# Kernel tuning notes

Hardware: AMD Instinct MI355X
Metric: run time of the kernel (lower is better)

The kernel has to match this reference:

```python
import jax, jax.numpy as jnp
import numpy as np

SIM_THRESHOLD = 0.7
EPS = 1e-8  # matches torch F.cosine_similarity eps

Q, M, D, C = 4096, 65536, 384, 128


def setup_inputs() -> dict:
    key = jax.random.key(0)
    k1, k2, k3 = jax.random.split(key, 3)
    query_embeddings = jax.random.normal(k1, (Q, D), dtype=jnp.float32)
    memory_embeddings = jax.random.normal(k2, (M, D), dtype=jnp.float32)
    # per-example one-hot-ish label vectors [M, C]
    memory_labels = jax.random.uniform(k3, (M, C), dtype=jnp.float32)
    return {
        "query_embeddings": query_embeddings,
        "memory_embeddings": memory_embeddings,
        "memory_labels": memory_labels,
    }


def _l2_normalize(x):
    n = jnp.sqrt(jnp.sum(x * x, axis=-1, keepdims=True))
    return x / jnp.maximum(n, EPS)


def reference(query_embeddings, memory_embeddings, memory_labels):
    # cosine similarity matrix [Q, M] via normalized GEMM
    qn = _l2_normalize(query_embeddings)          # [Q, D]
    mn = _l2_normalize(memory_embeddings)         # [M, D]
    sims = jnp.einsum("qd,md->qm", qn, mn)        # [Q, M]
    max_sim = jnp.max(sims, axis=1)               # [Q]
    max_idx = jnp.argmax(sims, axis=1)            # [Q]
    picked = memory_labels[max_idx]               # [Q, C] gather
    C_ = memory_labels.shape[1]
    uniform = jnp.full((1, C_), 1.0 / C_, dtype=picked.dtype)
    predictions = jnp.where((max_sim > SIM_THRESHOLD)[:, None], picked, uniform)
    return predictions
```

## Files before the change

### kernel.cpp

```cpp
#include <hip/hip_runtime.h>
#include <math.h>

#define QN 4096
#define MN 65536
#define DN 384
#define CN 128
#define NCHUNK 64
#define MROWS_PER_CHUNK (MN / NCHUNK)
#define MT_PER (MROWS_PER_CHUNK / 64)

#define LROW 400
#define LCHUNKS 25
#define BTILE_B (64 * LROW)
#define GTILE_B (64 * DN)

typedef __attribute__((ext_vector_type(8))) int i32x8;
typedef __attribute__((ext_vector_type(4))) int i32x4;
typedef __attribute__((ext_vector_type(4))) float f32x4;

__device__ __forceinline__ unsigned char f2fp8(float f) {
  return (unsigned char)(__builtin_amdgcn_cvt_pk_fp8_f32(f, 0.f, 0, false) & 0xff);
}

__device__ __forceinline__ void async16(const void* g, void* l) {
  __builtin_amdgcn_global_load_lds(
      (const __attribute__((address_space(1))) unsigned int*)g,
      (__attribute__((address_space(3))) unsigned int*)l, 16, 0, 0);
}

__global__ __launch_bounds__(256) void nrm_kernel(const float* __restrict__ qe,
                                                  const float* __restrict__ me,
                                                  unsigned char* __restrict__ yq,
                                                  unsigned char* __restrict__ ym) {
  const int row = blockIdx.x * 4 + (threadIdx.x >> 6);
  const int lane = threadIdx.x & 63;
  const float* xr;
  unsigned char* yr;
  if (row < QN) {
    xr = qe + (size_t)row * DN;
    yr = yq + (size_t)row * DN;
  } else {
    xr = me + (size_t)(row - QN) * DN;
    yr = ym + (size_t)(row - QN) * DN;
  }
  float v[6];
  float ss = 0.f;
#pragma unroll
  for (int i = 0; i < 6; ++i) {
    v[i] = xr[lane + i * 64];
    ss += v[i] * v[i];
  }
#pragma unroll
  for (int m = 1; m < 64; m <<= 1) ss += __shfl_xor(ss, m);
  const float scale = 1.0f / fmaxf(sqrtf(ss), 1e-8f);
#pragma unroll
  for (int i = 0; i < 6; ++i) yr[lane + i * 64] = f2fp8(v[i] * scale);
}

__global__ __launch_bounds__(256, 2) void gemm_max_kernel(
    const unsigned char* __restrict__ qn8, const unsigned char* __restrict__ mn8,
    float* __restrict__ pmax) {
  __shared__ unsigned char Bs[2 * BTILE_B];
  __shared__ float smax[2][128];

  const int tid = threadIdx.x;
  const int wave = tid >> 6, lane = tid & 63;
  const int wr = wave >> 1, wc = wave & 1;
  const int quad = lane >> 4, l16 = lane & 15;

  const int bid = blockIdx.y * gridDim.x + blockIdx.x;
  const int xcd = bid & 7;
  const int j = bid >> 3;
  const int ychunk = (xcd << 3) | (j >> 5);
  const int qrow0 = (j & 31) * 128;
  const int mchunk0 = ychunk * MROWS_PER_CHUNK;

  float rmax[16];
#pragma unroll
  for (int i = 0; i < 16; ++i) rmax[i] = -3.0e38f;

  {
    const unsigned char* abase = qn8 + (size_t)qrow0 * DN;
#pragma unroll
    for (int i = 0; i < 12; ++i) {
      const int ci = i * 256 + tid;
      const int row = ci / LCHUNKS;
      const int c16 = ci - row * LCHUNKS;
      const int sc = (c16 < 24) ? c16 : 0;
      async16(abase + row * DN + sc * 16, &Bs[(i * 256 + wave * 64) * 16]);
    }
    if (wave < 2) {
      const int ci = 3072 + wave * 64 + lane;
      const int row = ci / LCHUNKS;
      const int c16 = ci - row * LCHUNKS;
      const int sc = (c16 < 24) ? c16 : 0;
      async16(abase + row * DN + sc * 16, &Bs[(3072 + wave * 64) * 16]);
    }
  }
  __syncthreads();
  i32x8 afr[3][4];
#pragma unroll
  for (int kc = 0; kc < 3; ++kc)
#pragma unroll
    for (int rt = 0; rt < 4; ++rt) {
      const unsigned char* p = &Bs[(wr * 64 + rt * 16 + l16) * LROW + kc * 128];
      i32x4 lo = *(const i32x4*)&p[(quad * 2 + 0) * 16];
      i32x4 hi = *(const i32x4*)&p[(quad * 2 + 1) * 16];
      afr[kc][rt][0] = lo[0]; afr[kc][rt][1] = lo[1];
      afr[kc][rt][2] = lo[2]; afr[kc][rt][3] = lo[3];
      afr[kc][rt][4] = hi[0]; afr[kc][rt][5] = hi[1];
      afr[kc][rt][6] = hi[2]; afr[kc][rt][7] = hi[3];
    }
  __syncthreads();

  int srcoff[7];
#pragma unroll
  for (int i = 0; i < 6; ++i) {
    const int ci = i * 256 + tid;
    const int row = ci / LCHUNKS;
    const int c16 = ci - row * LCHUNKS;
    const int sc = (c16 < 24) ? c16 : 0;
    srcoff[i] = row * DN + sc * 16;
  }
  {
    const int ci = 1536 + lane;
    const int row = ci / LCHUNKS;
    const int c16 = ci - row * LCHUNKS;
    const int sc = (c16 < 24) ? c16 : 0;
    srcoff[6] = row * DN + sc * 16;
  }

  const unsigned char* bchunk = mn8 + (size_t)mchunk0 * DN;
#pragma unroll
  for (int i = 0; i < 6; ++i)
    async16(bchunk + srcoff[i], &Bs[(i * 256 + wave * 64) * 16]);
  if (wave == 0) async16(bchunk + srcoff[6], &Bs[1536 * 16]);

  const int c_lo = (quad * 2 + 0) * 16;
  const int c_hi = (quad * 2 + 1) * 16;

#pragma unroll 1
  for (int mt = 0; mt < MT_PER; ++mt) {
    __syncthreads();
    const unsigned char* cur = &Bs[(mt & 1) * BTILE_B];
    if (mt + 1 < MT_PER) {
      unsigned char* nxt = &Bs[((mt + 1) & 1) * BTILE_B];
      const unsigned char* nb = bchunk + (size_t)(mt + 1) * GTILE_B;
#pragma unroll
      for (int i = 0; i < 6; ++i)
        async16(nb + srcoff[i], &nxt[(i * 256 + wave * 64) * 16]);
      if (wave == 0) async16(nb + srcoff[6], &nxt[1536 * 16]);
    }

    i32x8 bfr[3][2];
#pragma unroll
    for (int kc = 0; kc < 3; ++kc)
#pragma unroll
      for (int ct = 0; ct < 2; ++ct) {
        const unsigned char* p =
            &cur[(wc * 32 + ct * 16 + l16) * LROW + kc * 128];
        i32x4 lo = *(const i32x4*)&p[c_lo];
        i32x4 hi = *(const i32x4*)&p[c_hi];
        bfr[kc][ct][0] = lo[0]; bfr[kc][ct][1] = lo[1];
        bfr[kc][ct][2] = lo[2]; bfr[kc][ct][3] = lo[3];
        bfr[kc][ct][4] = hi[0]; bfr[kc][ct][5] = hi[1];
        bfr[kc][ct][6] = hi[2]; bfr[kc][ct][7] = hi[3];
      }

    f32x4 acc[4][2];
#pragma unroll
    for (int rt = 0; rt < 4; ++rt)
#pragma unroll
      for (int ct = 0; ct < 2; ++ct) acc[rt][ct] = (f32x4){0.f, 0.f, 0.f, 0.f};

#pragma unroll
    for (int kc = 0; kc < 3; ++kc)
#pragma unroll
      for (int rt = 0; rt < 4; ++rt)
#pragma unroll
        for (int ct = 0; ct < 2; ++ct)
          acc[rt][ct] = __builtin_amdgcn_mfma_scale_f32_16x16x128_f8f6f4(
              afr[kc][rt], bfr[kc][ct], acc[rt][ct], 0, 0,
              0, 0x7f7f7f7f, 0, 0x7f7f7f7f);

#pragma unroll
    for (int rt = 0; rt < 4; ++rt)
#pragma unroll
      for (int r = 0; r < 4; ++r) {
        const float v = fmaxf(acc[rt][0][r], acc[rt][1][r]);
        rmax[rt * 4 + r] = fmaxf(rmax[rt * 4 + r], v);
      }
  }

#pragma unroll
  for (int i = 0; i < 16; ++i) {
    float v = rmax[i];
    v = fmaxf(v, __shfl_xor(v, 1));
    v = fmaxf(v, __shfl_xor(v, 2));
    v = fmaxf(v, __shfl_xor(v, 4));
    v = fmaxf(v, __shfl_xor(v, 8));
    rmax[i] = v;
  }
  if (l16 == 0) {
#pragma unroll
    for (int rt = 0; rt < 4; ++rt)
#pragma unroll
      for (int r = 0; r < 4; ++r)
        smax[wc][wr * 64 + rt * 16 + quad * 4 + r] = rmax[rt * 4 + r];
  }
  __syncthreads();
  if (tid < 128) {
    const float v = fmaxf(smax[0][tid], smax[1][tid]);
    pmax[(size_t)(qrow0 + tid) * NCHUNK + ychunk] = v;
  }
}

__global__ __launch_bounds__(256) void decide_kernel(
    const float* __restrict__ pmax, const float* __restrict__ qe,
    const float* __restrict__ me, const float* __restrict__ labels,
    float* __restrict__ out) {
  const int q = blockIdx.x;
  const int t = threadIdx.x;
  __shared__ float smx;
  if (t < 64) {
    float v = pmax[(size_t)q * NCHUNK + t];
#pragma unroll
    for (int m = 1; m < 64; m <<= 1) v = fmaxf(v, __shfl_xor(v, m));
    if (t == 0) smx = v;
  }
  __syncthreads();
  if (smx <= 0.5f) {
    if (t < CN) out[(size_t)q * CN + t] = 1.0f / 128.0f;
    return;
  }
  __shared__ float sred[256];
  __shared__ int sidx[256];
  __shared__ float wsum[4];
  const float* qr = qe + (size_t)q * DN;
  float ss = 0.f;
  for (int i = t; i < DN; i += 256) ss += qr[i] * qr[i];
#pragma unroll
  for (int m = 1; m < 64; m <<= 1) ss += __shfl_xor(ss, m);
  if ((t & 63) == 0) wsum[t >> 6] = ss;
  __syncthreads();
  const float qnorm = fmaxf(sqrtf(wsum[0] + wsum[1] + wsum[2] + wsum[3]), 1e-8f);

  float best = -3.0e38f;
  int bidx = 0x7fffffff;
  for (int j = t; j < MN; j += 256) {
    const float* mr = me + (size_t)j * DN;
    float dot = 0.f, ms = 0.f;
    for (int k = 0; k < DN; ++k) {
      float a = qr[k], b = mr[k];
      dot += a * b;
      ms += b * b;
    }
    const float sim = dot / (qnorm * fmaxf(sqrtf(ms), 1e-8f));
    if (sim > best) { best = sim; bidx = j; }
  }
  sred[t] = best;
  sidx[t] = bidx;
  __syncthreads();
  for (int s = 128; s > 0; s >>= 1) {
    if (t < s) {
      const float ov = sred[t + s];
      const int oi = sidx[t + s];
      if (ov > sred[t] || (ov == sred[t] && oi < sidx[t])) {
        sred[t] = ov;
        sidx[t] = oi;
      }
    }
    __syncthreads();
  }
  const float mx = sred[0];
  const int mi = sidx[0];
  if (t < CN)
    out[(size_t)q * CN + t] =
        (mx > 0.7f) ? labels[(size_t)mi * CN + t] : (1.0f / 128.0f);
}

extern "C" void kernel_launch(void* const* d_in, const int* in_sizes, int n_in,
                              void* d_out, int out_size, void* d_ws,
                              size_t ws_size, hipStream_t stream) {
  const float* qe = (const float*)d_in[0];
  const float* me = (const float*)d_in[1];
  const float* lb = (const float*)d_in[2];
  float* out = (float*)d_out;

  char* ws = (char*)d_ws;
  const size_t OFF_QN = 0;
  const size_t OFF_MN = OFF_QN + (size_t)QN * DN;
  const size_t OFF_PMAX = OFF_MN + (size_t)MN * DN;
  unsigned char* qn8 = (unsigned char*)(ws + OFF_QN);
  unsigned char* mn8 = (unsigned char*)(ws + OFF_MN);
  float* pmax = (float*)(ws + OFF_PMAX);

  nrm_kernel<<<(QN + MN) / 4, 256, 0, stream>>>(qe, me, qn8, mn8);
  gemm_max_kernel<<<dim3(QN / 128, NCHUNK), 256, 0, stream>>>(qn8, mn8, pmax);
  decide_kernel<<<QN, 256, 0, stream>>>(pmax, qe, me, lb, out);
}
```

Before: 258.5 us.

## Load B fragments directly from global memory, dropping LDS double buffering

The GEMM-max kernel no longer stages memory-embedding tiles through double-buffered shared memory with async global-to-LDS copies and barriers. Each lane now reads its 32-byte fp8 B fragments straight from global memory every iteration, so shared memory shrinks to a single A tile. This removes the per-tile __syncthreads and the LDS traffic, but it gives up explicit prefetch overlap. It also drops sharing of B loads between the two wave rows, so each B element is fetched twice from cache.

```diff
diff --git a/kernel.cpp b/kernel.cpp
--- a/kernel.cpp
+++ b/kernel.cpp
@@ -8,11 +8,10 @@
 #define NCHUNK 64
 #define MROWS_PER_CHUNK (MN / NCHUNK)
 #define MT_PER (MROWS_PER_CHUNK / 64)
+#define GTILE_B (64 * DN)
 
 #define LROW 400
 #define LCHUNKS 25
-#define BTILE_B (64 * LROW)
-#define GTILE_B (64 * DN)
 
 typedef __attribute__((ext_vector_type(8))) int i32x8;
 typedef __attribute__((ext_vector_type(4))) int i32x4;
@@ -60,7 +59,7 @@
 __global__ __launch_bounds__(256, 2) void gemm_max_kernel(
     const unsigned char* __restrict__ qn8, const unsigned char* __restrict__ mn8,
     float* __restrict__ pmax) {
-  __shared__ unsigned char Bs[2 * BTILE_B];
+  __shared__ unsigned char As[128 * LROW];
   __shared__ float smax[2][128];
 
   const int tid = threadIdx.x;
@@ -87,14 +86,14 @@
       const int row = ci / LCHUNKS;
       const int c16 = ci - row * LCHUNKS;
       const int sc = (c16 < 24) ? c16 : 0;
-      async16(abase + row * DN + sc * 16, &Bs[(i * 256 + wave * 64) * 16]);
+      async16(abase + row * DN + sc * 16, &As[(i * 256 + wave * 64) * 16]);
     }
     if (wave < 2) {
       const int ci = 3072 + wave * 64 + lane;
       const int row = ci / LCHUNKS;
       const int c16 = ci - row * LCHUNKS;
       const int sc = (c16 < 24) ? c16 : 0;
-      async16(abase + row * DN + sc * 16, &Bs[(3072 + wave * 64) * 16]);
+      async16(abase + row * DN + sc * 16, &As[(3072 + wave * 64) * 16]);
     }
   }
   __syncthreads();
@@ -103,7 +102,7 @@
   for (int kc = 0; kc < 3; ++kc)
 #pragma unroll
     for (int rt = 0; rt < 4; ++rt) {
-      const unsigned char* p = &Bs[(wr * 64 + rt * 16 + l16) * LROW + kc * 128];
+      const unsigned char* p = &As[(wr * 64 + rt * 16 + l16) * LROW + kc * 128];
       i32x4 lo = *(const i32x4*)&p[(quad * 2 + 0) * 16];
       i32x4 hi = *(const i32x4*)&p[(quad * 2 + 1) * 16];
       afr[kc][rt][0] = lo[0]; afr[kc][rt][1] = lo[1];
@@ -111,61 +110,19 @@
       afr[kc][rt][4] = hi[0]; afr[kc][rt][5] = hi[1];
       afr[kc][rt][6] = hi[2]; afr[kc][rt][7] = hi[3];
     }
-  __syncthreads();
-
-  int srcoff[7];
-#pragma unroll
-  for (int i = 0; i < 6; ++i) {
-    const int ci = i * 256 + tid;
-    const int row = ci / LCHUNKS;
-    const int c16 = ci - row * LCHUNKS;
-    const int sc = (c16 < 24) ? c16 : 0;
-    srcoff[i] = row * DN + sc * 16;
-  }
-  {
-    const int ci = 1536 + lane;
-    const int row = ci / LCHUNKS;
-    const int c16 = ci - row * LCHUNKS;
-    const int sc = (c16 < 24) ? c16 : 0;
-    srcoff[6] = row * DN + sc * 16;
-  }
-
-  const unsigned char* bchunk = mn8 + (size_t)mchunk0 * DN;
-#pragma unroll
-  for (int i = 0; i < 6; ++i)
-    async16(bchunk + srcoff[i], &Bs[(i * 256 + wave * 64) * 16]);
-  if (wave == 0) async16(bchunk + srcoff[6], &Bs[1536 * 16]);
-
-  const int c_lo = (quad * 2 + 0) * 16;
-  const int c_hi = (quad * 2 + 1) * 16;
+
+  const unsigned char* bl0 =
+      mn8 + (size_t)(mchunk0 + wc * 32 + l16) * DN + quad * 32;
+  const unsigned char* bl1 = bl0 + 16 * DN;
 
 #pragma unroll 1
   for (int mt = 0; mt < MT_PER; ++mt) {
-    __syncthreads();
-    const unsigned char* cur = &Bs[(mt & 1) * BTILE_B];
-    if (mt + 1 < MT_PER) {
-      unsigned char* nxt = &Bs[((mt + 1) & 1) * BTILE_B];
-      const unsigned char* nb = bchunk + (size_t)(mt + 1) * GTILE_B;
-#pragma unroll
-      for (int i = 0; i < 6; ++i)
-        async16(nb + srcoff[i], &nxt[(i * 256 + wave * 64) * 16]);
-      if (wave == 0) async16(nb + srcoff[6], &nxt[1536 * 16]);
-    }
-
     i32x8 bfr[3][2];
 #pragma unroll
-    for (int kc = 0; kc < 3; ++kc)
-#pragma unroll
-      for (int ct = 0; ct < 2; ++ct) {
-        const unsigned char* p =
-            &cur[(wc * 32 + ct * 16 + l16) * LROW + kc * 128];
-        i32x4 lo = *(const i32x4*)&p[c_lo];
-        i32x4 hi = *(const i32x4*)&p[c_hi];
-        bfr[kc][ct][0] = lo[0]; bfr[kc][ct][1] = lo[1];
-        bfr[kc][ct][2] = lo[2]; bfr[kc][ct][3] = lo[3];
-        bfr[kc][ct][4] = hi[0]; bfr[kc][ct][5] = hi[1];
-        bfr[kc][ct][6] = hi[2]; bfr[kc][ct][7] = hi[3];
-      }
+    for (int kc = 0; kc < 3; ++kc) {
+      bfr[kc][0] = *(const i32x8*)(bl0 + kc * 128);
+      bfr[kc][1] = *(const i32x8*)(bl1 + kc * 128);
+    }
 
     f32x4 acc[4][2];
 #pragma unroll
@@ -190,6 +147,9 @@
         const float v = fmaxf(acc[rt][0][r], acc[rt][1][r]);
         rmax[rt * 4 + r] = fmaxf(rmax[rt * 4 + r], v);
       }
+
+    bl0 += GTILE_B;
+    bl1 += GTILE_B;
   }
 
 #pragma unroll
```

Result: slower. 369.3 us (+42.9%).
